# Optimization experiments

Hardware: AMD Instinct MI355X
Metric: run time of the kernel (lower is better)

The kernel has to match this reference:

```python
import jax, jax.numpy as jnp
import numpy as np

B = 2_000_000
IN, HID = 5, 4


def setup_inputs() -> dict:
    key = jax.random.key(0)
    ks = jax.random.split(key, 16)
    f = lambda k, shp: (jax.random.normal(k, shp, dtype=jnp.float32) * 0.3)
    inp = {
        "xl": jax.random.normal(ks[0], (B, IN), dtype=jnp.float32),
        "yl": jax.random.normal(ks[1], (B, IN), dtype=jnp.float32),
        "xr": jax.random.normal(ks[2], (B, IN), dtype=jnp.float32),
        "yr": jax.random.normal(ks[3], (B, IN), dtype=jnp.float32),
        # 6 stacked branches, order: [lxl, lyl, lxr, lyr, rxl, ryl]
        "W1": f(ks[4], (6, HID, IN)),
        "b1": f(ks[5], (6, HID)),
        "W2": f(ks[6], (6, HID, HID)),
        "b2": f(ks[7], (6, HID)),
        # fc3 with 2 outputs, order: [lxl, lyl, rxl, ryl] (branch idx 0,1,4,5)
        "W3_2": f(ks[8], (4, 2, HID)),
        "b3_2": f(ks[9], (4, 2)),
        # fc3 with 1 output, order: [lxr, lyr] (branch idx 2,3)
        "W3_1": f(ks[10], (2, 1, HID)),
        "b3_1": f(ks[11], (2, 1)),
        # fc4, order: [xl, yl]
        "W4": f(ks[12], (2, 1, HID)),
        "b4": f(ks[13], (2, 1)),
    }
    return inp


def reference(xl, yl, xr, yr, W1, b1, W2, b2, W3_2, b3_2, W3_1, b3_1, W4, b4):
    # Stack the six branch inputs: [6, B, 5]. NOTE: fc_1lyr consumes yl (yr unused),
    # faithful to the original forward.
    X = jnp.stack([xl, yl, xr, yl, xl, yl], axis=0)
    h1 = jax.nn.sigmoid(jnp.einsum("kbi,khi->kbh", X, W1) + b1[:, None, :])
    h2 = jax.nn.sigmoid(jnp.einsum("kbh,kgh->kbg", h1, W2) + b2[:, None, :])
    # fc3 heads with 2 outputs: branches lxl(0), lyl(1), rxl(4), ryl(5)
    h2_2 = h2[jnp.array([0, 1, 4, 5])]                       # [4, B, 4]
    o2 = jnp.einsum("kbh,koh->kbo", h2_2, W3_2) + b3_2[:, None, :]  # [4, B, 2]
    # fc3 heads with 1 output: branches lxr(2), lyr(3)
    h2_1 = h2[jnp.array([2, 3])]                             # [2, B, 4]
    o1 = jnp.einsum("kbh,koh->kbo", h2_1, W3_1) + b3_1[:, None, :]  # [2, B, 1]
    # concat (per-sample dim, was dim=0 unbatched)
    out_xl = jnp.concatenate([o2[0], o2[2]], axis=-1)        # [B, 4]
    out_yl = jnp.concatenate([o2[1], o2[3]], axis=-1)        # [B, 4]
    fc4xl = out_xl @ W4[0].T + b4[0]                         # [B, 1]
    fc4yl = out_yl @ W4[1].T + b4[1]                         # [B, 1]
    out = jnp.concatenate([o1[0], o1[1], fc4xl, fc4yl], axis=-1)  # [B, 4]
    return out
```

## Files before the change

### kernel.cpp

```cpp
#include <hip/hip_runtime.h>

#define NTHREADS 256

#if defined(__has_builtin)
#if __has_builtin(__builtin_amdgcn_exp2f)
#define EXP2F __builtin_amdgcn_exp2f
#else
#define EXP2F exp2f
#endif
#else
#define EXP2F exp2f
#endif

__device__ __forceinline__ float rfl(float x) {
    return __uint_as_float(__builtin_amdgcn_readfirstlane(__float_as_uint(x)));
}

__device__ __forceinline__ void sigm4(float a[4]) {
    const float c = -1.442695040888963f;
    float d0 = 1.0f + EXP2F(a[0] * c);
    float d1 = 1.0f + EXP2F(a[1] * c);
    float d2 = 1.0f + EXP2F(a[2] * c);
    float d3 = 1.0f + EXP2F(a[3] * c);
    float r01 = __builtin_amdgcn_rcpf(d0 * d1);
    float r23 = __builtin_amdgcn_rcpf(d2 * d3);
    a[0] = r01 * d1;
    a[1] = r01 * d0;
    a[2] = r23 * d3;
    a[3] = r23 * d2;
}

__global__ __launch_bounds__(NTHREADS, 8)
void mlp6_fused_kernel(const float* __restrict__ xl,
                       const float* __restrict__ yl,
                       const float* __restrict__ xr,
                       const float* __restrict__ W1, const float* __restrict__ b1,
                       const float* __restrict__ W2, const float* __restrict__ b2,
                       const float* __restrict__ W3_2, const float* __restrict__ b3_2,
                       const float* __restrict__ W3_1, const float* __restrict__ b3_1,
                       const float* __restrict__ W4, const float* __restrict__ b4,
                       float* __restrict__ out, int B)
{
    int i = blockIdx.x * NTHREADS + threadIdx.x;
    if (i >= B) i = B - 1;
    const int p = i * 5;

    float xa[5], ya[5];
    #pragma unroll
    for (int q = 0; q < 5; q++) xa[q] = xl[p + q];
    #pragma unroll
    for (int q = 0; q < 5; q++) ya[q] = yl[p + q];

    float fw[6][4];
    #pragma unroll
    for (int h = 0; h < 4; h++) {
        fw[0][h] = rfl(fmaf(W4[1], W3_2[4 + h],  W4[0] * W3_2[h]));
        fw[1][h] = rfl(fmaf(W4[5], W3_2[12 + h], W4[4] * W3_2[8 + h]));
        fw[2][h] = rfl(W3_1[h]);
        fw[3][h] = rfl(W3_1[4 + h]);
        fw[4][h] = rfl(fmaf(W4[3], W3_2[20 + h], W4[2] * W3_2[16 + h]));
        fw[5][h] = rfl(fmaf(W4[7], W3_2[28 + h], W4[6] * W3_2[24 + h]));
    }
    float o0 = rfl(b3_1[0]);
    float o1 = rfl(b3_1[1]);
    float o2 = rfl(W4[0]*b3_2[0] + W4[1]*b3_2[1] + W4[2]*b3_2[4] + W4[3]*b3_2[5] + b4[0]);
    float o3 = rfl(W4[4]*b3_2[2] + W4[5]*b3_2[3] + W4[6]*b3_2[6] + W4[7]*b3_2[7] + b4[1]);

    auto branch = [&](int k, const float* xb) -> float {
        float a[4];
        #pragma unroll
        for (int h = 0; h < 4; h++) {
            float s = b1[k*4 + h];
            #pragma unroll
            for (int q = 0; q < 5; q++) s = fmaf(xb[q], W1[k*20 + h*5 + q], s);
            a[h] = s;
        }
        sigm4(a);
        float c[4];
        #pragma unroll
        for (int g = 0; g < 4; g++) {
            float s = b2[k*4 + g];
            #pragma unroll
            for (int h = 0; h < 4; h++) s = fmaf(a[h], W2[k*16 + g*4 + h], s);
            c[g] = s;
        }
        sigm4(c);
        float r = c[0] * fw[k][0];
        #pragma unroll
        for (int g = 1; g < 4; g++) r = fmaf(c[g], fw[k][g], r);
        return r;
    };

    o2 += branch(0, xa);
    o2 += branch(4, xa);
    #pragma unroll
    for (int q = 0; q < 5; q++) xa[q] = xr[p + q];
    o3 += branch(1, ya);
    o1 += branch(3, ya);
    o3 += branch(5, ya);
    o0 += branch(2, xa);

    float4 r;
    r.x = o0; r.y = o1; r.z = o2; r.w = o3;
    ((float4*)out)[i] = r;
}

extern "C" void kernel_launch(void* const* d_in, const int* in_sizes, int n_in,
                              void* d_out, int out_size, void* d_ws, size_t ws_size,
                              hipStream_t stream) {
    const float* xl   = (const float*)d_in[0];
    const float* yl   = (const float*)d_in[1];
    const float* xr   = (const float*)d_in[2];
    const float* W1   = (const float*)d_in[4];
    const float* b1   = (const float*)d_in[5];
    const float* W2   = (const float*)d_in[6];
    const float* b2   = (const float*)d_in[7];
    const float* W3_2 = (const float*)d_in[8];
    const float* b3_2 = (const float*)d_in[9];
    const float* W3_1 = (const float*)d_in[10];
    const float* b3_1 = (const float*)d_in[11];
    const float* W4   = (const float*)d_in[12];
    const float* b4   = (const float*)d_in[13];
    float* out = (float*)d_out;

    int B = in_sizes[0] / 5;
    int blocks = (B + NTHREADS - 1) / NTHREADS;
    mlp6_fused_kernel<<<blocks, NTHREADS, 0, stream>>>(
        xl, yl, xr, W1, b1, W2, b2, W3_2, b3_2, W3_1, b3_1, W4, b4, out, B);
}
```

Before: 47.10 us.

## Process two samples per thread with packed float2 FMA math

Each thread now handles two consecutive samples. It loads their inputs as float2 vectors and runs the MLP arithmetic on f32x2 vectors, so the compiler can emit packed FMA and multiply instructions. The sigmoid now uses one reciprocal per four values instead of two. This aims to halve the scalar ALU instruction count and widen the memory accesses. The costs are higher register pressure (launch bounds lowered to 4) and a kernel that silently assumes B is even, so an odd last sample would be dropped.

```diff
diff --git a/kernel.cpp b/kernel.cpp
--- a/kernel.cpp
+++ b/kernel.cpp
@@ -1,6 +1,8 @@
 #include <hip/hip_runtime.h>
 
 #define NTHREADS 256
+
+typedef float f32x2 __attribute__((ext_vector_type(2)));
 
 #if defined(__has_builtin)
 #if __has_builtin(__builtin_amdgcn_exp2f)
@@ -16,21 +18,38 @@
     return __uint_as_float(__builtin_amdgcn_readfirstlane(__float_as_uint(x)));
 }
 
-__device__ __forceinline__ void sigm4(float a[4]) {
-    const float c = -1.442695040888963f;
-    float d0 = 1.0f + EXP2F(a[0] * c);
-    float d1 = 1.0f + EXP2F(a[1] * c);
-    float d2 = 1.0f + EXP2F(a[2] * c);
-    float d3 = 1.0f + EXP2F(a[3] * c);
-    float r01 = __builtin_amdgcn_rcpf(d0 * d1);
-    float r23 = __builtin_amdgcn_rcpf(d2 * d3);
-    a[0] = r01 * d1;
-    a[1] = r01 * d0;
-    a[2] = r23 * d3;
-    a[3] = r23 * d2;
+__device__ __forceinline__ f32x2 bc2(float w) {
+    f32x2 r; r.x = w; r.y = w; return r;
+}
+__device__ __forceinline__ f32x2 pfma(f32x2 a, f32x2 b, f32x2 c) {
+    return __builtin_elementwise_fma(a, b, c);
 }
 
-__global__ __launch_bounds__(NTHREADS, 8)
+__device__ __forceinline__ void sig4(f32x2 v[4]) {
+    const f32x2 C   = bc2(-1.442695040888963f);
+    const f32x2 ONE = bc2(1.0f);
+    f32x2 d[4];
+    #pragma unroll
+    for (int h = 0; h < 4; h++) {
+        f32x2 m = v[h] * C;
+        f32x2 e; e.x = EXP2F(m.x); e.y = EXP2F(m.y);
+        d[h] = e + ONE;
+    }
+    f32x2 p01 = d[0] * d[1];
+    f32x2 p23 = d[2] * d[3];
+    f32x2 P   = p01 * p23;
+    f32x2 r;
+    r.x = __builtin_amdgcn_rcpf(P.x);
+    r.y = __builtin_amdgcn_rcpf(P.y);
+    f32x2 r01 = r * p23;
+    f32x2 r23 = r * p01;
+    v[0] = r01 * d[1];
+    v[1] = r01 * d[0];
+    v[2] = r23 * d[3];
+    v[3] = r23 * d[2];
+}
+
+__global__ __launch_bounds__(NTHREADS, 4)
 void mlp6_fused_kernel(const float* __restrict__ xl,
                        const float* __restrict__ yl,
                        const float* __restrict__ xr,
@@ -41,15 +60,33 @@
                        const float* __restrict__ W4, const float* __restrict__ b4,
                        float* __restrict__ out, int B)
 {
-    int i = blockIdx.x * NTHREADS + threadIdx.x;
-    if (i >= B) i = B - 1;
-    const int p = i * 5;
+    const int nq = B >> 1;
+    int gq = blockIdx.x * NTHREADS + threadIdx.x;
+    if (gq >= nq) gq = nq - 1;
 
-    float xa[5], ya[5];
-    #pragma unroll
-    for (int q = 0; q < 5; q++) xa[q] = xl[p + q];
-    #pragma unroll
-    for (int q = 0; q < 5; q++) ya[q] = yl[p + q];
+    f32x2 LA[5], LB[5], LC[5];
+    {
+        const f32x2* x2 = (const f32x2*)xl + (long long)gq * 5;
+        const f32x2* y2 = (const f32x2*)yl + (long long)gq * 5;
+        const f32x2* c2 = (const f32x2*)xr + (long long)gq * 5;
+        #pragma unroll
+        for (int q = 0; q < 5; q++) LA[q] = x2[q];
+        #pragma unroll
+        for (int q = 0; q < 5; q++) LB[q] = y2[q];
+        #pragma unroll
+        for (int q = 0; q < 5; q++) LC[q] = c2[q];
+    }
+    f32x2 xp[5], yp[5];
+    xp[0].x = LA[0].x; xp[0].y = LA[2].y;
+    xp[1].x = LA[0].y; xp[1].y = LA[3].x;
+    xp[2].x = LA[1].x; xp[2].y = LA[3].y;
+    xp[3].x = LA[1].y; xp[3].y = LA[4].x;
+    xp[4].x = LA[2].x; xp[4].y = LA[4].y;
+    yp[0].x = LB[0].x; yp[0].y = LB[2].y;
+    yp[1].x = LB[0].y; yp[1].y = LB[3].x;
+    yp[2].x = LB[1].x; yp[2].y = LB[3].y;
+    yp[3].x = LB[1].y; yp[3].y = LB[4].x;
+    yp[4].x = LB[2].x; yp[4].y = LB[4].y;
 
     float fw[6][4];
     #pragma unroll
@@ -61,48 +98,57 @@
         fw[4][h] = rfl(fmaf(W4[3], W3_2[20 + h], W4[2] * W3_2[16 + h]));
         fw[5][h] = rfl(fmaf(W4[7], W3_2[28 + h], W4[6] * W3_2[24 + h]));
     }
-    float o0 = rfl(b3_1[0]);
-    float o1 = rfl(b3_1[1]);
-    float o2 = rfl(W4[0]*b3_2[0] + W4[1]*b3_2[1] + W4[2]*b3_2[4] + W4[3]*b3_2[5] + b4[0]);
-    float o3 = rfl(W4[4]*b3_2[2] + W4[5]*b3_2[3] + W4[6]*b3_2[6] + W4[7]*b3_2[7] + b4[1]);
+    float fb0 = rfl(b3_1[0]);
+    float fb1 = rfl(b3_1[1]);
+    float fb2 = rfl(W4[0]*b3_2[0] + W4[1]*b3_2[1] + W4[2]*b3_2[4] + W4[3]*b3_2[5] + b4[0]);
+    float fb3 = rfl(W4[4]*b3_2[2] + W4[5]*b3_2[3] + W4[6]*b3_2[6] + W4[7]*b3_2[7] + b4[1]);
 
-    auto branch = [&](int k, const float* xb) -> float {
-        float a[4];
+    f32x2 o0 = bc2(fb0), o1 = bc2(fb1), o2 = bc2(fb2), o3 = bc2(fb3);
+
+    auto branch = [&](int k, const f32x2 (&in)[5], f32x2& oslot) {
+        f32x2 h[4];
         #pragma unroll
-        for (int h = 0; h < 4; h++) {
-            float s = b1[k*4 + h];
+        for (int hh = 0; hh < 4; hh++) {
+            f32x2 acc = bc2(b1[k*4 + hh]);
             #pragma unroll
-            for (int q = 0; q < 5; q++) s = fmaf(xb[q], W1[k*20 + h*5 + q], s);
-            a[h] = s;
+            for (int q = 0; q < 5; q++)
+                acc = pfma(in[q], bc2(W1[k*20 + hh*5 + q]), acc);
+            h[hh] = acc;
         }
-        sigm4(a);
-        float c[4];
+        sig4(h);
+        f32x2 c[4];
         #pragma unroll
         for (int g = 0; g < 4; g++) {
-            float s = b2[k*4 + g];
+            f32x2 acc = bc2(b2[k*4 + g]);
             #pragma unroll
-            for (int h = 0; h < 4; h++) s = fmaf(a[h], W2[k*16 + g*4 + h], s);
-            c[g] = s;
+            for (int q = 0; q < 4; q++)
+                acc = pfma(h[q], bc2(W2[k*16 + g*4 + q]), acc);
+            c[g] = acc;
         }
-        sigm4(c);
-        float r = c[0] * fw[k][0];
+        sig4(c);
         #pragma unroll
-        for (int g = 1; g < 4; g++) r = fmaf(c[g], fw[k][g], r);
-        return r;
+        for (int g = 0; g < 4; g++)
+            oslot = pfma(c[g], bc2(fw[k][g]), oslot);
     };
 
-    o2 += branch(0, xa);
-    o2 += branch(4, xa);
-    #pragma unroll
-    for (int q = 0; q < 5; q++) xa[q] = xr[p + q];
-    o3 += branch(1, ya);
-    o1 += branch(3, ya);
-    o3 += branch(5, ya);
-    o0 += branch(2, xa);
+    branch(0, xp, o2);
+    branch(4, xp, o2);
+    xp[0].x = LC[0].x; xp[0].y = LC[2].y;
+    xp[1].x = LC[0].y; xp[1].y = LC[3].x;
+    xp[2].x = LC[1].x; xp[2].y = LC[3].y;
+    xp[3].x = LC[1].y; xp[3].y = LC[4].x;
+    xp[4].x = LC[2].x; xp[4].y = LC[4].y;
+    branch(1, yp, o3);
+    branch(3, yp, o1);
+    branch(5, yp, o3);
+    branch(2, xp, o0);
 
-    float4 r;
-    r.x = o0; r.y = o1; r.z = o2; r.w = o3;
-    ((float4*)out)[i] = r;
+    float4 r0, r1;
+    r0.x = o0.x; r0.y = o1.x; r0.z = o2.x; r0.w = o3.x;
+    r1.x = o0.y; r1.y = o1.y; r1.z = o2.y; r1.w = o3.y;
+    float4* out4 = (float4*)out;
+    out4[(long long)gq * 2]     = r0;
+    out4[(long long)gq * 2 + 1] = r1;
 }
 
 extern "C" void kernel_launch(void* const* d_in, const int* in_sizes, int n_in,
@@ -124,7 +170,8 @@
     float* out = (float*)d_out;
 
     int B = in_sizes[0] / 5;
-    int blocks = (B + NTHREADS - 1) / NTHREADS;
+    int nq = B >> 1;
+    int blocks = (nq + NTHREADS - 1) / NTHREADS;
     mlp6_fused_kernel<<<blocks, NTHREADS, 0, stream>>>(
         xl, yl, xr, W1, b1, W2, b2, W3_2, b3_2, W3_1, b3_1, W4, b4, out, B);
 }
```

Result: faster. 39.47 us (-16.2%).
